# Kernel optimization log

Measured on AMD Instinct MI355X. Metric: run time of the kernel, lower is better.

## Reference

```python
import jax, jax.numpy as jnp
import numpy as np

WS = (7, 7, 7)
DIM = 384
HEADS = 12
N = WS[0] * WS[1] * WS[2]  # 343 tokens per window
B = 128                    # batch * num_windows
NW = 32                    # number of distinct shift masks (b % nw == 0)
TABLE = (2 * WS[0] - 1) * (2 * WS[1] - 1) * (2 * WS[2] - 1)  # 2197


def _rel_position_index(ws):
    # Faithful port of the torch __init__ index construction (3D case).
    coords = np.stack(np.meshgrid(np.arange(ws[0]), np.arange(ws[1]), np.arange(ws[2]), indexing='ij'))
    cf = coords.reshape(3, -1)                      # [3, n]
    rc = cf[:, :, None] - cf[:, None, :]            # [3, n, n]
    rc = rc.transpose(1, 2, 0).copy()               # [n, n, 3]
    rc[:, :, 0] += ws[0] - 1
    rc[:, :, 1] += ws[1] - 1
    rc[:, :, 2] += ws[2] - 1
    rc[:, :, 0] *= (2 * ws[1] - 1) * (2 * ws[2] - 1)
    rc[:, :, 1] *= 2 * ws[2] - 1
    return rc.sum(-1).astype(np.int32)              # [n, n] in [0, TABLE)


def setup_inputs() -> dict:
    key = jax.random.key(0)
    ks = jax.random.split(key, 6)
    x = jax.random.normal(ks[0], (B, N, DIM), dtype=jnp.float32)
    w_qkv = jax.random.normal(ks[1], (3 * DIM, DIM), dtype=jnp.float32) * 0.02
    bias_table = jax.random.normal(ks[2], (TABLE, HEADS), dtype=jnp.float32) * 0.02
    w_proj = jax.random.normal(ks[3], (DIM, DIM), dtype=jnp.float32) * 0.02
    b_proj = jnp.zeros((DIM,), dtype=jnp.float32)
    # Shift mask: 0 where attention allowed, -100 where blocked (Swin convention).
    mask = jnp.where(jax.random.uniform(ks[4], (NW, N, N)) < 0.9, 0.0, -100.0).astype(jnp.float32)
    q_global = jnp.zeros((1, 1), dtype=jnp.float32)  # unused by forward
    rel_index = jnp.asarray(_rel_position_index(WS))
    return {"x": x, "D": 28, "H": 28, "W": 28, "mask": mask, "q_global": q_global,
            "w_qkv": w_qkv, "bias_table": bias_table, "w_proj": w_proj,
            "b_proj": b_proj, "rel_index": rel_index}


def reference(x, D, H, W, mask, q_global, w_qkv, bias_table, w_proj, b_proj, rel_index):
    b, n, c = x.shape
    h = HEADS
    d = c // h
    scale = d ** -0.5
    # qkv projection (no bias, qkv_bias=False)
    qkv = jnp.einsum('bnc,fc->bnf', x, w_qkv).reshape(b, n, 3, h, d)
    qkv = qkv.transpose(2, 0, 3, 1, 4)               # [3, b, h, n, d]
    q, k, v = qkv[0], qkv[1], qkv[2]
    attn = jnp.einsum('bhid,bhjd->bhij', q * scale, k)  # [b, h, n, n]
    # relative position bias gather: [n*n] -> [n, n, h] -> [h, n, n]
    bias = bias_table[rel_index.reshape(-1)].reshape(n, n, h).transpose(2, 0, 1)
    attn = attn + bias[None]
    if mask is not None:
        nw = mask.shape[0]
        attn = attn.reshape(b // nw, nw, h, n, n) + mask[None, :, None]
        attn = attn.reshape(b, h, n, n)
    attn = jax.nn.softmax(attn, axis=-1)
    out = jnp.einsum('bhij,bhjd->bhid', attn, v)      # [b, h, n, d]
    out = out.transpose(0, 2, 1, 3).reshape(b, n, c)
    out = out @ w_proj.T + b_proj
    return out
```

## Files before the change

kernel.cpp:

```cpp
#include <hip/hip_runtime.h>
#include <hip/hip_fp16.h>
#include <math.h>

#define BATCH 128
#define NTOK  343
#define NPAD  352
#define CDIM  384
#define NH    12
#define DH    32
#define NWIN  32
#define MTOK  (BATCH*NTOK)
#define NN    (NTOK*NTOK)
#define QKVF  (3*CDIM)
#define KSTR  40
#define VSTR  360
#define PSTR  106
#define MBW   11
#define BTI   22
#define BJT   22
#define BSWT  (BTI*BJT*256)

#define LOG2E 1.4426950408889634f

typedef float    f32x4 __attribute__((ext_vector_type(4)));
typedef _Float16 half8 __attribute__((ext_vector_type(8)));
typedef _Float16 half4 __attribute__((ext_vector_type(4)));

#define LDS_K   (NPAD*KSTR)
#define LDS_V   (DH*VSTR)
#define LDS_P   (16*PSTR)
#define LDS_TOT (LDS_K + LDS_V + 8*LDS_P)

#define NX    (MTOK*CDIM)
#define NWQ   (QKVF*CDIM)
#define NWP   (CDIM*CDIM)
#define NXB   (NX/2048)
#define NWQB  (NWQ/2048)
#define NWPB  (NWP/2048)
#define NMKB  ((NWIN*NTOK+3)/4)
#define NBSB  ((BSWT+255)/256)
#define PREPB (NXB+NWQB+NWPB+NMKB+NBSB)

__device__ __forceinline__ void gl2lds16(const __half* g, __half* l) {
  __builtin_amdgcn_global_load_lds(
      (const __attribute__((address_space(1))) void*)g,
      (__attribute__((address_space(3))) void*)l,
      16, 0, 0);
}

__device__ __forceinline__ void cvt8(const float* in, __half* out, int i) {
  float4 a = *(const float4*)&in[i];
  float4 b = *(const float4*)&in[i + 4];
  half8 h;
  h[0] = (_Float16)a.x; h[1] = (_Float16)a.y; h[2] = (_Float16)a.z; h[3] = (_Float16)a.w;
  h[4] = (_Float16)b.x; h[5] = (_Float16)b.y; h[6] = (_Float16)b.z; h[7] = (_Float16)b.w;
  *(half8*)&out[i] = h;
}

__global__ __launch_bounds__(256) void prep_k(
    const float* __restrict__ x,      __half* __restrict__ xh,
    const float* __restrict__ wq,     __half* __restrict__ wqh,
    const float* __restrict__ wp,     __half* __restrict__ wph,
    const float* __restrict__ mask,   unsigned int* __restrict__ mbits,
    const int* __restrict__ rel_index, const float* __restrict__ table,
    __half* __restrict__ bias_sw) {
  const int blk = blockIdx.x;
  const int tid = threadIdx.x;

  if (blk < NXB) {
    int i = (blk * 256 + tid) * 8;
    if (i < NX) cvt8(x, xh, i);
    return;
  }
  if (blk < NXB + NWQB) {
    int i = ((blk - NXB) * 256 + tid) * 8;
    if (i < NWQ) cvt8(wq, wqh, i);
    return;
  }
  if (blk < NXB + NWQB + NWPB) {
    int i = ((blk - NXB - NWQB) * 256 + tid) * 8;
    if (i < NWP) cvt8(wp, wph, i);
    return;
  }
  if (blk < NXB + NWQB + NWPB + NMKB) {
    int row = (blk - NXB - NWQB - NWPB) * 4 + (tid >> 6);
    int lane = tid & 63;
    if (row >= NWIN * NTOK) return;
    const float* mr = mask + (size_t)row * NTOK;
#pragma unroll
    for (int seg = 0; seg < 6; ++seg) {
      int j = seg * 64 + lane;
      bool allowed = (j < NTOK) ? (mr[j] == 0.0f) : false;
      unsigned long long bits = __ballot(allowed);
      if (lane == 0) mbits[(size_t)row * MBW + seg*2] = (unsigned)bits;
      if (lane == 1 && seg*2 + 1 < MBW) mbits[(size_t)row * MBW + seg*2 + 1] = (unsigned)(bits >> 32);
    }
    return;
  }
  {
    int t = (blk - NXB - NWQB - NWPB - NMKB) * 256 + tid;
    if (t >= BSWT) return;
    int r  = t & 3;
    int lr = (t >> 2) & 15;
    int lg = (t >> 6) & 3;
    int jt = (t >> 8) % BJT;
    int ti = (t >> 8) / BJT;
    int i = ti * 16 + lg * 4 + r;
    int j = jt * 16 + lr;
    if (i < NTOK && j < NTOK) {
      int idx = rel_index[i * NTOK + j];
#pragma unroll
      for (int hh = 0; hh < NH; ++hh)
        bias_sw[(size_t)hh * BSWT + t] = __float2half(table[idx * NH + hh] * LOG2E);
    } else {
      __half pad = __float2half(-1000.0f);
#pragma unroll
      for (int hh = 0; hh < NH; ++hh)
        bias_sw[(size_t)hh * BSWT + t] = pad;
    }
  }
}

template<int EPI>
__global__ __launch_bounds__(256) void gemm_mfma_k(
    const __half* __restrict__ Ah, const __half* __restrict__ Bh,
    const float* __restrict__ bias, void* __restrict__ Cv) {
  __shared__ __half As[1024 * 8];
  __shared__ __half Bs[1024 * 8];
  const int tid  = threadIdx.x;
  const int lane = tid & 63, wave = tid >> 6;
  const int lr = lane & 15, lg = lane >> 4;
  const int wr = wave >> 1, wc = wave & 1;

  const int nwg = gridDim.x * gridDim.y;
  const int flat = blockIdx.y * gridDim.x + blockIdx.x;
  const int q = nwg >> 3, rr = nwg & 7;
  const int xcd = flat & 7, lid = flat >> 3;
  const int swz = (xcd < rr ? xcd * (q + 1) : rr * (q + 1) + (xcd - rr) * q) + lid;
  const int n0 = (swz % gridDim.x) * 128;
  const int m0 = (swz / gridDim.x) * 128;
  const int KD = 384;

  f32x4 acc[4][4];
#pragma unroll
  for (int i = 0; i < 4; ++i)
#pragma unroll
    for (int j = 0; j < 4; ++j) acc[i][j] = (f32x4){0.f, 0.f, 0.f, 0.f};

  for (int k0 = 0; k0 < KD; k0 += 64) {
#pragma unroll
    for (int i = 0; i < 4; ++i) {
      int cb = wave * 256 + i * 64;
      int c  = cb + lane;
      int row = c & 127, kg = c >> 7;
      gl2lds16(&Ah[(size_t)(m0 + row) * KD + k0 + kg * 8], &As[cb * 8]);
      gl2lds16(&Bh[(size_t)(n0 + row) * KD + k0 + kg * 8], &Bs[cb * 8]);
    }
    __syncthreads();

#pragma unroll
    for (int kk = 0; kk < 2; ++kk) {
      const int kg = lg + kk * 4;
      half8 af[4], bf[4];
#pragma unroll
      for (int t = 0; t < 4; ++t) {
        af[t] = *(const half8*)&As[(kg * 128 + wr * 64 + t * 16 + lr) * 8];
        bf[t] = *(const half8*)&Bs[(kg * 128 + wc * 64 + t * 16 + lr) * 8];
      }
#pragma unroll
      for (int mi = 0; mi < 4; ++mi)
#pragma unroll
        for (int ni = 0; ni < 4; ++ni)
          acc[mi][ni] = __builtin_amdgcn_mfma_f32_16x16x32_f16(af[mi], bf[ni], acc[mi][ni], 0, 0, 0);
    }
    __syncthreads();
  }

#pragma unroll
  for (int mi = 0; mi < 4; ++mi) {
#pragma unroll
    for (int r = 0; r < 4; ++r) {
      int m = m0 + wr * 64 + mi * 16 + lg * 4 + r;
#pragma unroll
      for (int ni = 0; ni < 4; ++ni) {
        int f = n0 + wc * 64 + ni * 16 + lr;
        float v = acc[mi][ni][r];
        if (EPI == 0) {
          if (f < CDIM) v *= (0.17677669529663687f * LOG2E);
          ((__half*)Cv)[(size_t)m * QKVF + f] = __float2half(v);
        } else {
          ((float*)Cv)[(size_t)m * CDIM + f] = v + bias[f];
        }
      }
    }
  }
}

__global__ __launch_bounds__(512, 1) void attn_k(
    const __half* __restrict__ qkvh, const __half* __restrict__ bias_sw,
    const unsigned int* __restrict__ mbits, __half* __restrict__ av) {
  extern __shared__ __half smem[];
  __half* Ks = smem;
  __half* Vt = smem + LDS_K;
  const int tid  = threadIdx.x;
  const int wave = tid >> 6, lane = tid & 63;
  const int lr   = lane & 15, lg = lane >> 4;
  __half* Pw = smem + LDS_K + LDS_V + wave * LDS_P;

  const int bh = blockIdx.x;
  const int b  = bh / NH, h = bh - b * NH;
  const int w  = b & (NWIN - 1);
  const size_t tbase = (size_t)b * NTOK;
  const int hoff = h * DH;

  for (int idx = tid; idx < NPAD * 4; idx += 512) {
    int j = idx >> 2, off = (idx & 3) << 3;
    half8 val = {0,0,0,0,0,0,0,0};
    if (j < NTOK) val = *reinterpret_cast<const half8*>(&qkvh[(tbase + j) * QKVF + CDIM + hoff + off]);
    *reinterpret_cast<half8*>(&Ks[j * KSTR + off]) = val;
  }
  for (int idx = tid; idx < NPAD * 4; idx += 512) {
    int j = idx >> 2, off = (idx & 3) << 3;
    if (j < NTOK) {
      union { float4 f; __half h[8]; } u;
      u.f = *reinterpret_cast<const float4*>(&qkvh[(tbase + j) * QKVF + 2 * CDIM + hoff + off]);
#pragma unroll
      for (int uu = 0; uu < 8; ++uu) Vt[(off + uu) * VSTR + j] = u.h[uu];
    } else {
#pragma unroll
      for (int uu = 0; uu < 8; ++uu) Vt[(off + uu) * VSTR + j] = __float2half(0.f);
    }
  }
  __syncthreads();

  const __half* bias_h = bias_sw + (size_t)h * BSWT;
  const unsigned int* mb_w = mbits + (size_t)w * NTOK * MBW;
  const int lgofs = lg * 64 + lr * 4;

  for (int i0 = wave * 16; i0 < NPAD; i0 += 128) {
    int qrow = min(i0 + lr, NTOK - 1);
    half8 qa = *reinterpret_cast<const half8*>(&qkvh[(tbase + qrow) * QKVF + hoff + lg * 8]);

    int il[4];
#pragma unroll
    for (int r = 0; r < 4; ++r) il[r] = min(i0 + lg * 4 + r, NTOK - 1);
    const __half* bias_t = bias_h + (size_t)(i0 >> 4) * (BJT * 256) + lgofs;

    f32x4 o0 = {0.f, 0.f, 0.f, 0.f}, o1 = {0.f, 0.f, 0.f, 0.f};
    float sm[4] = {0.f, 0.f, 0.f, 0.f};
    const f32x4 zf = {0.f, 0.f, 0.f, 0.f};

#pragma unroll
    for (int c = 0; c < 4; ++c) {
      const int njt = (c < 3) ? 6 : 4;
      const int nkt = (c < 3) ? 3 : 2;

      f32x4 s[6];
#pragma unroll
      for (int jl_ = 0; jl_ < njt; ++jl_) {
        int jt = c * 6 + jl_;
        half8 kb = *reinterpret_cast<const half8*>(&Ks[(jt * 16 + lr) * KSTR + lg * 8]);
        s[jl_] = __builtin_amdgcn_mfma_f32_16x16x32_f16(qa, kb, zf, 0, 0, 0);
      }

#pragma unroll
      for (int jl_ = 0; jl_ < njt; ++jl_) {
        int jt = c * 6 + jl_;
        half4 bt = *(const half4*)&bias_t[jt * 256];
        unsigned sh = (unsigned)(((jt & 1) << 4) + lr);
#pragma unroll
        for (int r = 0; r < 4; ++r) {
          unsigned mwv = mb_w[il[r] * MBW + (jt >> 1)];
          float madd = ((mwv >> sh) & 1u) ? 0.f : (-100.f * LOG2E);
          float p = exp2f(s[jl_][r] + (float)bt[r] + madd);
          sm[r] += p;
          Pw[(lg * 4 + r) * PSTR + jl_ * 16 + lr] = __float2half(p);
        }
      }
      asm volatile("s_waitcnt lgkmcnt(0)" ::: "memory");
      __builtin_amdgcn_sched_barrier(0);

#pragma unroll
      for (int ktl = 0; ktl < nkt; ++ktl) {
        int ktg = c * 3 + ktl;
        half8 pa  = *reinterpret_cast<const half8*>(&Pw[lr * PSTR + ktl * 32 + lg * 8]);
        half8 vb0 = *reinterpret_cast<const half8*>(&Vt[lr * VSTR + ktg * 32 + lg * 8]);
        half8 vb1 = *reinterpret_cast<const half8*>(&Vt[(16 + lr) * VSTR + ktg * 32 + lg * 8]);
        o0 = __builtin_amdgcn_mfma_f32_16x16x32_f16(pa, vb0, o0, 0, 0, 0);
        o1 = __builtin_amdgcn_mfma_f32_16x16x32_f16(pa, vb1, o1, 0, 0, 0);
      }
      __builtin_amdgcn_sched_barrier(0);
    }

#pragma unroll
    for (int off = 1; off <= 8; off <<= 1)
#pragma unroll
      for (int r = 0; r < 4; ++r) sm[r] += __shfl_xor(sm[r], off);

#pragma unroll
    for (int r = 0; r < 4; ++r) {
      int i = i0 + lg * 4 + r;
      if (i < NTOK) {
        float inv = 1.f / sm[r];
        size_t ob = ((size_t)b * NTOK + i) * CDIM + hoff;
        av[ob + lr]      = __float2half(o0[r] * inv);
        av[ob + 16 + lr] = __float2half(o1[r] * inv);
      }
    }
  }
}

extern "C" void kernel_launch(void* const* d_in, const int* in_sizes, int n_in,
                              void* d_out, int out_size, void* d_ws, size_t ws_size,
                              hipStream_t stream) {
  const float* x          = (const float*)d_in[0];
  const float* mask       = (const float*)d_in[4];
  const float* w_qkv      = (const float*)d_in[6];
  const float* bias_table = (const float*)d_in[7];
  const float* w_proj     = (const float*)d_in[8];
  const float* b_proj     = (const float*)d_in[9];
  const int*   rel_index  = (const int*)d_in[10];
  float* out = (float*)d_out;

  __half* qkvh   = (__half*)d_ws;
  __half* avb    = qkvh + (size_t)MTOK * QKVF;
  __half* xh     = avb;
  __half* bias_sw = avb + (size_t)MTOK * CDIM;
  unsigned int* mbits = (unsigned int*)(bias_sw + (size_t)NH * BSWT);
  __half* wqkvh  = (__half*)(mbits + (size_t)NWIN * NTOK * MBW);
  __half* wprojh = wqkvh + (size_t)QKVF * CDIM;

  prep_k<<<PREPB, 256, 0, stream>>>(x, xh, w_qkv, wqkvh, w_proj, wprojh,
                                    mask, mbits, rel_index, bias_table, bias_sw);

  gemm_mfma_k<0><<<dim3(QKVF / 128, MTOK / 128), 256, 0, stream>>>(
      xh, wqkvh, nullptr, qkvh);

  (void)hipFuncSetAttribute((const void*)attn_k,
                            hipFuncAttributeMaxDynamicSharedMemorySize, LDS_TOT * 2);
  attn_k<<<BATCH * NH, 512, LDS_TOT * 2, stream>>>(qkvh, bias_sw, mbits, avb);

  gemm_mfma_k<1><<<dim3(CDIM / 128, MTOK / 128), 256, 0, stream>>>(
      avb, wprojh, b_proj, out);
}
```

Baseline: 268.8 us.

## Transpose QK^T MFMA output so each lane owns one query row

Swaps the MFMA operands so the score tile comes out transposed, with each lane holding four consecutive keys for a single query row. The mask word is then loaded once per key tile instead of four times, and P is written to LDS as one packed half4 store instead of four scalar stores. The row-sum reduction shrinks to two cross-lane shuffles plus a broadcast, and the bias swizzle and P stride are changed to match the new layout. Getting the index mapping exactly right is the risk, and the extra shuffle in the epilogue adds a little work.

```diff
diff --git a/kernel.cpp b/kernel.cpp
--- a/kernel.cpp
+++ b/kernel.cpp
@@ -14,7 +14,7 @@
 #define QKVF  (3*CDIM)
 #define KSTR  40
 #define VSTR  360
-#define PSTR  106
+#define PSTR  108
 #define MBW   11
 #define BTI   22
 #define BJT   22
@@ -105,8 +105,8 @@
     int lg = (t >> 6) & 3;
     int jt = (t >> 8) % BJT;
     int ti = (t >> 8) / BJT;
-    int i = ti * 16 + lg * 4 + r;
-    int j = jt * 16 + lr;
+    int i = ti * 16 + lr;
+    int j = jt * 16 + lg * 4 + r;
     if (i < NTOK && j < NTOK) {
       int idx = rel_index[i * NTOK + j];
 #pragma unroll
@@ -241,13 +241,12 @@
     int qrow = min(i0 + lr, NTOK - 1);
     half8 qa = *reinterpret_cast<const half8*>(&qkvh[(tbase + qrow) * QKVF + hoff + lg * 8]);
 
-    int il[4];
-#pragma unroll
-    for (int r = 0; r < 4; ++r) il[r] = min(i0 + lg * 4 + r, NTOK - 1);
+    const int il = min(i0 + lr, NTOK - 1);
+    const unsigned int* mb_i = mb_w + il * MBW;
     const __half* bias_t = bias_h + (size_t)(i0 >> 4) * (BJT * 256) + lgofs;
 
     f32x4 o0 = {0.f, 0.f, 0.f, 0.f}, o1 = {0.f, 0.f, 0.f, 0.f};
-    float sm[4] = {0.f, 0.f, 0.f, 0.f};
+    float sm = 0.f;
     const f32x4 zf = {0.f, 0.f, 0.f, 0.f};
 
 #pragma unroll
@@ -260,22 +259,26 @@
       for (int jl_ = 0; jl_ < njt; ++jl_) {
         int jt = c * 6 + jl_;
         half8 kb = *reinterpret_cast<const half8*>(&Ks[(jt * 16 + lr) * KSTR + lg * 8]);
-        s[jl_] = __builtin_amdgcn_mfma_f32_16x16x32_f16(qa, kb, zf, 0, 0, 0);
+        s[jl_] = __builtin_amdgcn_mfma_f32_16x16x32_f16(kb, qa, zf, 0, 0, 0);
       }
 
 #pragma unroll
       for (int jl_ = 0; jl_ < njt; ++jl_) {
         int jt = c * 6 + jl_;
         half4 bt = *(const half4*)&bias_t[jt * 256];
-        unsigned sh = (unsigned)(((jt & 1) << 4) + lr);
+        unsigned mwv = mb_i[jt >> 1];
+        unsigned sh = (unsigned)(((jt & 1) << 4) + lg * 4);
+        float p[4];
 #pragma unroll
         for (int r = 0; r < 4; ++r) {
-          unsigned mwv = mb_w[il[r] * MBW + (jt >> 1)];
-          float madd = ((mwv >> sh) & 1u) ? 0.f : (-100.f * LOG2E);
-          float p = exp2f(s[jl_][r] + (float)bt[r] + madd);
-          sm[r] += p;
-          Pw[(lg * 4 + r) * PSTR + jl_ * 16 + lr] = __float2half(p);
+          float madd = ((mwv >> (sh + r)) & 1u) ? 0.f : (-100.f * LOG2E);
+          p[r] = exp2f(s[jl_][r] + (float)bt[r] + madd);
+          sm += p[r];
         }
+        half4 hv;
+        hv[0] = (_Float16)p[0]; hv[1] = (_Float16)p[1];
+        hv[2] = (_Float16)p[2]; hv[3] = (_Float16)p[3];
+        *(half4*)&Pw[lr * PSTR + jl_ * 16 + lg * 4] = hv;
       }
       asm volatile("s_waitcnt lgkmcnt(0)" ::: "memory");
       __builtin_amdgcn_sched_barrier(0);
@@ -292,16 +295,15 @@
       __builtin_amdgcn_sched_barrier(0);
     }
 
-#pragma unroll
-    for (int off = 1; off <= 8; off <<= 1)
-#pragma unroll
-      for (int r = 0; r < 4; ++r) sm[r] += __shfl_xor(sm[r], off);
+    sm += __shfl_xor(sm, 16);
+    sm += __shfl_xor(sm, 32);
 
 #pragma unroll
     for (int r = 0; r < 4; ++r) {
       int i = i0 + lg * 4 + r;
       if (i < NTOK) {
-        float inv = 1.f / sm[r];
+        float smr = __shfl(sm, (lane & 48) | (lg * 4 + r));
+        float inv = 1.f / smr;
         size_t ob = ((size_t)b * NTOK + i) * CDIM + hoff;
         av[ob + lr]      = __float2half(o0[r] * inv);
         av[ob + 16 + lr] = __float2half(o1[r] * inv);
```

Measured after the change: 261.0 us. 2.9% less time.
